# Performance work log

Hardware: AMD Instinct MI355X
Metric: run time of the kernel (lower is better)

## Reference

```python
import jax, jax.numpy as jnp
import numpy as np

N_Q_HEADS = 16
N_KV_HEADS = 4
HEAD_DIM = 64
GROUPS = N_Q_HEADS // N_KV_HEADS


def apply_rope(xq, xk, cos, sin):
    # xq: [B,S,Hq,D], xk: [B,S,Hkv,D]; cos/sin: [S, D/2]
    def rot(t):
        tr = t[..., 0::2]
        ti = t[..., 1::2]
        c = cos[None, :, None, :]
        s = sin[None, :, None, :]
        out_r = tr * c - ti * s
        out_i = tr * s + ti * c
        # interleave back: [..., D/2, 2] -> [..., D]
        return jnp.stack([out_r, out_i], axis=-1).reshape(t.shape)
    return rot(xq), rot(xk)


def setup_inputs() -> dict:
    key = jax.random.key(0)
    ks = jax.random.split(key, 8)
    B, S, DIM = 2, 2048, 1024
    x = jax.random.normal(ks[0], (B, S, DIM), jnp.float32)
    # RoPE frequencies (llama-style): theta_i = 10000^(-2i/D), angles = pos * theta
    inv_freq = 1.0 / (10000.0 ** (jnp.arange(0, HEAD_DIM, 2, dtype=jnp.float32) / HEAD_DIM))
    angles = jnp.arange(S, dtype=jnp.float32)[:, None] * inv_freq[None, :]  # [S, D/2]
    freqs_cos = jnp.cos(angles)
    freqs_sin = jnp.sin(angles)
    # additive causal mask [1,1,S,S]
    neg = jnp.float32(-1e9)
    mask = jnp.where(jnp.tril(jnp.ones((S, S), bool)), 0.0, neg)[None, None]
    scale = 0.02
    wq = jax.random.normal(ks[1], (DIM, N_Q_HEADS * HEAD_DIM), jnp.float32) * scale
    wk = jax.random.normal(ks[2], (DIM, N_KV_HEADS * HEAD_DIM), jnp.float32) * scale
    wv = jax.random.normal(ks[3], (DIM, N_KV_HEADS * HEAD_DIM), jnp.float32) * scale
    wo = jax.random.normal(ks[4], (DIM, DIM), jnp.float32) * scale
    return {"x": x, "start_pos": 0, "freqs_cos": freqs_cos, "freqs_sin": freqs_sin,
            "mask": mask, "wq": wq, "wk": wk, "wv": wv, "wo": wo}


def reference(x, start_pos, freqs_cos, freqs_sin, mask, wq, wk, wv, wo):
    B, S, DIM = x.shape
    xq = (x @ wq).reshape(B, S, N_Q_HEADS, HEAD_DIM)
    xk = (x @ wk).reshape(B, S, N_KV_HEADS, HEAD_DIM)
    xv = (x @ wv).reshape(B, S, N_KV_HEADS, HEAD_DIM)
    xq, xk = apply_rope(xq, xk, freqs_cos, freqs_sin)
    # seq_len > 1: prefill path, no KV-cache read. repeat_kv: expand kv heads by GROUPS.
    keys = jnp.repeat(xk, GROUPS, axis=2)    # [B,S,Hq,D]
    values = jnp.repeat(xv, GROUPS, axis=2)
    q = xq.transpose(0, 2, 1, 3)             # [B,H,S,D]
    k = keys.transpose(0, 2, 1, 3)
    v = values.transpose(0, 2, 1, 3)
    scores = jnp.einsum('bhqd,bhkd->bhqk', q, k) / jnp.sqrt(jnp.float32(HEAD_DIM))
    scores = scores + mask
    probs = jax.nn.softmax(scores, axis=-1)
    attn = jnp.einsum('bhqk,bhkd->bhqd', probs, v)  # [B,H,S,D]
    attn = attn.transpose(0, 2, 1, 3).reshape(B, S, DIM)
    return attn @ wo
```

## Files before the change

kernel.cpp:

```cpp
#include <hip/hip_runtime.h>

typedef __bf16 bf16_t;
typedef __bf16 bf16x8 __attribute__((ext_vector_type(8)));
typedef __bf16 bf16x4 __attribute__((ext_vector_type(4)));
typedef float f32x4 __attribute__((ext_vector_type(4)));
typedef short short4v __attribute__((ext_vector_type(4)));

#if __has_builtin(__builtin_amdgcn_exp2f)
#define EXP2F __builtin_amdgcn_exp2f
#else
#define EXP2F exp2f
#endif

#define BATCH 2
#define SEQ   2048
#define DIM   1024
#define NQH   16
#define NKVH  4
#define HD    64
#define ROWS  (BATCH*SEQ)
#define QKVN  1536
#define QSCALE 0.1803368801111f

static __device__ __forceinline__ short4v as_s4(bf16x4 v) {
    union { bf16x4 b; short4v s; } u; u.b = v; return u.s;
}

static __device__ __forceinline__ void gld16(const bf16_t* g, bf16_t* l) {
    __builtin_amdgcn_global_load_lds((const __attribute__((address_space(1))) void*)g,
                                     (__attribute__((address_space(3))) void*)l,
                                     16, 0, 0);
}

__global__ __launch_bounds__(256) void cast_x_kernel(const float* __restrict__ x,
                                                     bf16_t* __restrict__ o) {
    size_t i = ((size_t)blockIdx.x * 256 + threadIdx.x) * 4;
    float4 v = *(const float4*)(x + i);
    bf16x4 r;
    r[0] = (bf16_t)v.x; r[1] = (bf16_t)v.y; r[2] = (bf16_t)v.z; r[3] = (bf16_t)v.w;
    *(bf16x4*)(o + i) = r;
}

__global__ __launch_bounds__(256) void transpose_w_all(const float* __restrict__ wq,
                                                       const float* __restrict__ wk,
                                                       const float* __restrict__ wv,
                                                       const float* __restrict__ wo,
                                                       bf16_t* __restrict__ WqkvT,
                                                       bf16_t* __restrict__ WoT) {
    int bid = blockIdx.x;
    const float* src; bf16_t* dst; int N, nt, kt2;
    if (bid < 256)      { src = wq; dst = WqkvT;                      N = 1024; int i = bid;       nt = i & 15; kt2 = i >> 4; }
    else if (bid < 320) { src = wk; dst = WqkvT + (size_t)1024*1024;  N = 256;  int i = bid - 256; nt = i & 3;  kt2 = i >> 2; }
    else if (bid < 384) { src = wv; dst = WqkvT + (size_t)1280*1024;  N = 256;  int i = bid - 320; nt = i & 3;  kt2 = i >> 2; }
    else                { src = wo; dst = WoT;                        N = 1024; int i = bid - 384; nt = i & 15; kt2 = i >> 4; }

    __shared__ float tile[64][65];
    int t = threadIdx.x;
    {
        int r = t >> 2, cb = (t & 3) * 16;
        const float* s = src + (size_t)(kt2 * 64 + r) * N + nt * 64 + cb;
#pragma unroll
        for (int j = 0; j < 16; j += 4) {
            float4 v = *(const float4*)(s + j);
            tile[r][cb + j + 0] = v.x; tile[r][cb + j + 1] = v.y;
            tile[r][cb + j + 2] = v.z; tile[r][cb + j + 3] = v.w;
        }
    }
    __syncthreads();
    {
        int n = t >> 2, kb = (t & 3) * 16;
        union { bf16_t h[16]; uint4 u[2]; } pk;
#pragma unroll
        for (int j = 0; j < 16; ++j) pk.h[j] = (bf16_t)tile[kb + j][n];
        bf16_t* d = dst + (size_t)(nt * 64 + n) * 1024 + kt2 * 64 + kb;
        ((uint4*)d)[0] = pk.u[0];
        ((uint4*)d)[1] = pk.u[1];
    }
}

__global__ __launch_bounds__(256, 2) void gemm_qkv_kernel(const bf16_t* __restrict__ A,
                                                          const bf16_t* __restrict__ Bt,
                                                          const float* __restrict__ fcos,
                                                          const float* __restrict__ fsin,
                                                          bf16_t* __restrict__ Qb,
                                                          bf16_t* __restrict__ Kb,
                                                          bf16_t* __restrict__ Vt) {
    const int K = 1024;
    __shared__ __align__(16) bf16_t As[128 * 32];
    __shared__ __align__(16) bf16_t Bs[128 * 32];
    int t = threadIdx.x;
    int w = t >> 6, L = t & 63, quad = L >> 4, l15 = L & 15;
    int wr = (w >> 1) * 64, wc = (w & 1) * 64;
    int bnb = blockIdx.x;
    int bn = bnb * 128, bm = blockIdx.y * 128;

    const bf16_t* Ag0 = A  + (size_t)(bm + w * 32 + (L >> 2)) * K + (L & 3) * 8;
    const bf16_t* Ag1 = Ag0 + (size_t)16 * K;
    const bf16_t* Bg0 = Bt + (size_t)(bn + w * 32 + (L >> 2)) * K + (L & 3) * 8;
    const bf16_t* Bg1 = Bg0 + (size_t)16 * K;
    bf16_t* Al = As + w * 1024;
    bf16_t* Bl = Bs + w * 1024;

    f32x4 acc[4][4] = {};

    for (int k0 = 0; k0 < K; k0 += 32) {
        __syncthreads();
        gld16(Ag0 + k0, Al);
        gld16(Ag1 + k0, Al + 512);
        gld16(Bg0 + k0, Bl);
        gld16(Bg1 + k0, Bl + 512);
        __syncthreads();

        bf16x8 a[4], b[4];
#pragma unroll
        for (int i = 0; i < 4; ++i) {
            a[i] = ((const bf16x8*)As)[(wr + 16 * i + l15) * 4 + quad];
            b[i] = ((const bf16x8*)Bs)[(wc + 16 * i + l15) * 4 + quad];
        }
#pragma unroll
        for (int i = 0; i < 4; ++i)
#pragma unroll
            for (int j = 0; j < 4; ++j)
                acc[i][j] = __builtin_amdgcn_mfma_f32_16x16x32_bf16(a[i], b[j], acc[i][j], 0, 0, 0);
    }

    int region = (bnb >= 10) ? 2 : (bnb >= 8) ? 1 : 0;
#pragma unroll
    for (int i = 0; i < 4; ++i) {
        int row0 = bm + wr + 16 * i + quad * 4;
        int b = row0 >> 11, s0 = row0 & 2047;
#pragma unroll
        for (int j = 0; j < 4; ++j) {
            int col = bn + wc + 16 * j + l15;
            if (region == 2) {
                int kvh = (col >> 6) - 20, d = col & 63;
                bf16x4 o;
#pragma unroll
                for (int r = 0; r < 4; ++r) o[r] = (bf16_t)acc[i][j][r];
                *(bf16x4*)(Vt + ((size_t)((b * NKVH + kvh) * HD + d)) * SEQ + s0) = o;
            } else {
                int d = col & 63, fi = d >> 1;
                int odd = col & 1;
#pragma unroll
                for (int r = 0; r < 4; ++r) {
                    int s = s0 + r;
                    float v = acc[i][j][r];
                    float p = __shfl_xor(v, 1);
                    float c = fcos[s * 32 + fi], sn = fsin[s * 32 + fi];
                    float o = odd ? (p * sn + v * c) : (v * c - p * sn);
                    if (region == 0) {
                        int h = col >> 6;
                        Qb[((size_t)((b * NQH + h) * SEQ + s)) * HD + d] = (bf16_t)(o * QSCALE);
                    } else {
                        int kvh = (col >> 6) - 16;
                        Kb[((size_t)((b * NKVH + kvh) * SEQ + s)) * HD + d] = (bf16_t)o;
                    }
                }
            }
        }
    }
}

__global__ __launch_bounds__(256, 2) void gemm_bt_kernel(const bf16_t* __restrict__ A,
                                                         const bf16_t* __restrict__ Bt,
                                                         float* __restrict__ C,
                                                         int M, int N, int K) {
    __shared__ __align__(16) bf16_t As[128 * 32];
    __shared__ __align__(16) bf16_t Bs[128 * 32];
    int t = threadIdx.x;
    int w = t >> 6, L = t & 63, quad = L >> 4, l15 = L & 15;
    int wr = (w >> 1) * 64, wc = (w & 1) * 64;
    int bn = blockIdx.x * 128, bm = blockIdx.y * 128;

    const bf16_t* Ag0 = A  + (size_t)(bm + w * 32 + (L >> 2)) * K + (L & 3) * 8;
    const bf16_t* Ag1 = Ag0 + (size_t)16 * K;
    const bf16_t* Bg0 = Bt + (size_t)(bn + w * 32 + (L >> 2)) * K + (L & 3) * 8;
    const bf16_t* Bg1 = Bg0 + (size_t)16 * K;
    bf16_t* Al = As + w * 1024;
    bf16_t* Bl = Bs + w * 1024;

    f32x4 acc[4][4] = {};

    for (int k0 = 0; k0 < K; k0 += 32) {
        __syncthreads();
        gld16(Ag0 + k0, Al);
        gld16(Ag1 + k0, Al + 512);
        gld16(Bg0 + k0, Bl);
        gld16(Bg1 + k0, Bl + 512);
        __syncthreads();

        bf16x8 a[4], b[4];
#pragma unroll
        for (int i = 0; i < 4; ++i) {
            a[i] = ((const bf16x8*)As)[(wr + 16 * i + l15) * 4 + quad];
            b[i] = ((const bf16x8*)Bs)[(wc + 16 * i + l15) * 4 + quad];
        }
#pragma unroll
        for (int i = 0; i < 4; ++i)
#pragma unroll
            for (int j = 0; j < 4; ++j)
                acc[i][j] = __builtin_amdgcn_mfma_f32_16x16x32_bf16(a[i], b[j], acc[i][j], 0, 0, 0);
    }

#pragma unroll
    for (int i = 0; i < 4; ++i) {
        int row = bm + wr + 16 * i + quad * 4;
#pragma unroll
        for (int j = 0; j < 4; ++j) {
            int col = bn + wc + 16 * j + l15;
            float* cp = C + (size_t)row * N + col;
#pragma unroll
            for (int r = 0; r < 4; ++r)
                cp[(size_t)r * N] = acc[i][j][r];
        }
    }
}

__global__ __launch_bounds__(512, 2) void attn_kernel(const bf16_t* __restrict__ Qb,
                                                      const bf16_t* __restrict__ Kb,
                                                      const bf16_t* __restrict__ Vt,
                                                      bf16_t* __restrict__ Ob) {
    int bq = blockIdx.x, h = blockIdx.y, b = blockIdx.z;
    int kv = h >> 2;
    int t = threadIdx.x, w = t >> 6, lane = t & 63, quad = lane >> 4, l15 = lane & 15;

    __shared__ __align__(16) bf16_t Ks[64 * 64];
    __shared__ __align__(16) bf16_t Vs[64 * 64];

    const bf16_t* Qbase = Qb + ((size_t)(b * NQH + h)) * SEQ * HD;
    const bf16_t* Kbase = Kb + ((size_t)(b * NKVH + kv)) * SEQ * HD;
    const bf16_t* Vbase = Vt + ((size_t)(b * NKVH + kv)) * HD * SEQ;

    int sm = t >> 3, spos = t & 7, skc = spos ^ (sm & 7);
    const bf16_t* ksrc = Kbase + (size_t)sm * HD + skc * 8;
    const bf16_t* vsrc = Vbase + (size_t)sm * SEQ + skc * 8;

#pragma unroll 1
    for (int ph = 0; ph < 2; ++ph) {
        int qt = ph ? (15 - bq) : bq;
        int Q0 = qt * 128;
        int wq = Q0 + 16 * w + l15;
        int myktmax = (Q0 + 16 * w + 15) >> 6;
        int ktmax = (Q0 + 127) >> 6;

        bf16x8 aq[2];
#pragma unroll
        for (int ks = 0; ks < 2; ++ks)
            aq[ks] = *(const bf16x8*)(Qbase + (size_t)wq * HD + ks * 32 + quad * 8);

        f32x4 acc_o[4] = {};
        float rs = 0.f;

        uint4 kpre = *(const uint4*)ksrc;
        uint4 vpre = *(const uint4*)vsrc;

        for (int kt = 0; kt <= ktmax; ++kt) {
            __syncthreads();
            ((uint4*)Ks)[t] = kpre;
            ((uint4*)Vs)[t] = vpre;
            __syncthreads();
            if (kt < ktmax) {
                kpre = *(const uint4*)(ksrc + (size_t)(kt + 1) * 64 * HD);
                vpre = *(const uint4*)(vsrc + (size_t)(kt + 1) * 64);
            }
            if (kt > myktmax) continue;

            f32x4 st[4];
#pragma unroll
            for (int x = 0; x < 4; ++x) {
                int key = 16 * x + l15;
                bf16x8 ak0 = ((const bf16x8*)Ks)[key * 8 + ((0 + quad) ^ (key & 7))];
                bf16x8 ak1 = ((const bf16x8*)Ks)[key * 8 + ((4 + quad) ^ (key & 7))];
                f32x4 z = {0.f, 0.f, 0.f, 0.f};
                z = __builtin_amdgcn_mfma_f32_16x16x32_bf16(ak0, aq[0], z, 0, 0, 0);
                z = __builtin_amdgcn_mfma_f32_16x16x32_bf16(ak1, aq[1], z, 0, 0, 0);
                st[x] = z;
            }

            short4v bp[4];
            if (kt == myktmax) {
                int kb = kt * 64 + quad * 4;
#pragma unroll
                for (int x = 0; x < 4; ++x) {
                    bf16x4 pb;
#pragma unroll
                    for (int r = 0; r < 4; ++r) {
                        float p = (kb + 16 * x + r <= wq) ? EXP2F(st[x][r]) : 0.f;
                        rs += p; pb[r] = (bf16_t)p;
                    }
                    bp[x] = as_s4(pb);
                }
            } else {
#pragma unroll
                for (int x = 0; x < 4; ++x) {
                    bf16x4 pb;
#pragma unroll
                    for (int r = 0; r < 4; ++r) {
                        float p = EXP2F(st[x][r]);
                        rs += p; pb[r] = (bf16_t)p;
                    }
                    bp[x] = as_s4(pb);
                }
            }

#pragma unroll
            for (int dt = 0; dt < 4; ++dt) {
                int d = 16 * dt + l15;
#pragma unroll
                for (int x = 0; x < 4; ++x) {
                    int pos = (2 * x + (quad >> 1)) ^ (d & 7);
                    bf16x4 av = *(const bf16x4*)(Vs + d * 64 + pos * 8 + (quad & 1) * 4);
                    acc_o[dt] = __builtin_amdgcn_mfma_f32_16x16x16bf16_1k(as_s4(av), bp[x], acc_o[dt], 0, 0, 0);
                }
            }
        }

        rs += __shfl_xor(rs, 16);
        rs += __shfl_xor(rs, 32);
        float rinv = 1.0f / rs;
        bf16_t* obase = Ob + (size_t)(b * SEQ + wq) * DIM + h * HD;
#pragma unroll
        for (int dt = 0; dt < 4; ++dt) {
            bf16x4 o;
#pragma unroll
            for (int r = 0; r < 4; ++r) o[r] = (bf16_t)(acc_o[dt][r] * rinv);
            *(bf16x4*)(obase + 16 * dt + quad * 4) = o;
        }
    }
}

extern "C" void kernel_launch(void* const* d_in, const int* in_sizes, int n_in,
                              void* d_out, int out_size, void* d_ws, size_t ws_size,
                              hipStream_t stream) {
    const float* x    = (const float*)d_in[0];
    const float* fcos = (const float*)d_in[2];
    const float* fsin = (const float*)d_in[3];
    const float* wq   = (const float*)d_in[5];
    const float* wk   = (const float*)d_in[6];
    const float* wv   = (const float*)d_in[7];
    const float* wo   = (const float*)d_in[8];
    float* out = (float*)d_out;

    char* ws = (char*)d_ws;
    bf16_t* Xb    = (bf16_t*)(ws + 0);
    bf16_t* Attnb = Xb;
    bf16_t* WqkvT = (bf16_t*)(ws + 8388608);
    bf16_t* WoT   = (bf16_t*)(ws + 11534336);
    bf16_t* Qb    = (bf16_t*)(ws + 13631488);
    bf16_t* Kb    = (bf16_t*)(ws + 22020096);
    bf16_t* Vt    = (bf16_t*)(ws + 24117248);

    cast_x_kernel<<<ROWS * DIM / 1024, 256, 0, stream>>>(x, Xb);
    transpose_w_all<<<640, 256, 0, stream>>>(wq, wk, wv, wo, WqkvT, WoT);

    gemm_qkv_kernel<<<dim3(QKVN / 128, ROWS / 128), 256, 0, stream>>>(Xb, WqkvT, fcos, fsin, Qb, Kb, Vt);

    attn_kernel<<<dim3(8, NQH, BATCH), 512, 0, stream>>>(Qb, Kb, Vt, Attnb);

    gemm_bt_kernel<<<dim3(DIM / 128, ROWS / 128), 256, 0, stream>>>(Attnb, WoT, out, ROWS, DIM, DIM);
}
```

Before: 187.5 us.

## Retile K/V into MFMA-ready tiles and use 32x32 MFMA in attention

The QKV projection epilogue now writes K and V in a pre-tiled 64-key block layout that matches the LDS fragment order. The attention kernel loads each tile with direct global-to-LDS copies. It uses 32x32x16 MFMA on 32-query wave tiles and exchanges P fragments across lane halves with shuffles. Both causal half-tiles (bq and 15-bq) are handled at once by splitting the 8 waves instead of two sequential phases. This is meant to cut LDS swizzle and register staging overhead and to improve MFMA efficiency. In exchange it adds cross-lane shuffles, and some waves idle on tiles past their causal limit.

```diff
diff --git a/kernel.cpp b/kernel.cpp
--- a/kernel.cpp
+++ b/kernel.cpp
@@ -4,7 +4,7 @@
 typedef __bf16 bf16x8 __attribute__((ext_vector_type(8)));
 typedef __bf16 bf16x4 __attribute__((ext_vector_type(4)));
 typedef float f32x4 __attribute__((ext_vector_type(4)));
-typedef short short4v __attribute__((ext_vector_type(4)));
+typedef float f32x16 __attribute__((ext_vector_type(16)));
 
 #if __has_builtin(__builtin_amdgcn_exp2f)
 #define EXP2F __builtin_amdgcn_exp2f
@@ -21,10 +21,6 @@
 #define ROWS  (BATCH*SEQ)
 #define QKVN  1536
 #define QSCALE 0.1803368801111f
-
-static __device__ __forceinline__ short4v as_s4(bf16x4 v) {
-    union { bf16x4 b; short4v s; } u; u.b = v; return u.s;
-}
 
 static __device__ __forceinline__ void gld16(const bf16_t* g, bf16_t* l) {
     __builtin_amdgcn_global_load_lds((const __attribute__((address_space(1))) void*)g,
@@ -134,10 +130,12 @@
             int col = bn + wc + 16 * j + l15;
             if (region == 2) {
                 int kvh = (col >> 6) - 20, d = col & 63;
+                int kt = s0 >> 6, kl = s0 & 63;
                 bf16x4 o;
 #pragma unroll
                 for (int r = 0; r < 4; ++r) o[r] = (bf16_t)acc[i][j][r];
-                *(bf16x4*)(Vt + ((size_t)((b * NKVH + kvh) * HD + d)) * SEQ + s0) = o;
+                *(bf16x4*)(Vt + ((size_t)((b * NKVH + kvh) * 32 + kt)) * 4096
+                              + ((kl >> 3) * 64 + d) * 8 + (kl & 7)) = o;
             } else {
                 int d = col & 63, fi = d >> 1;
                 int odd = col & 1;
@@ -153,7 +151,9 @@
                         Qb[((size_t)((b * NQH + h) * SEQ + s)) * HD + d] = (bf16_t)(o * QSCALE);
                     } else {
                         int kvh = (col >> 6) - 16;
-                        Kb[((size_t)((b * NKVH + kvh) * SEQ + s)) * HD + d] = (bf16_t)o;
+                        int kt = s >> 6, kl = s & 63;
+                        Kb[((size_t)((b * NKVH + kvh) * 32 + kt)) * 4096
+                           + ((d >> 3) * 64 + kl) * 8 + (d & 7)] = (bf16_t)o;
                     }
                 }
             }
@@ -216,117 +216,109 @@
     }
 }
 
-__global__ __launch_bounds__(512, 2) void attn_kernel(const bf16_t* __restrict__ Qb,
-                                                      const bf16_t* __restrict__ Kb,
-                                                      const bf16_t* __restrict__ Vt,
-                                                      bf16_t* __restrict__ Ob) {
+__global__ __launch_bounds__(512) void attn_kernel(const bf16_t* __restrict__ Qb,
+                                                   const bf16_t* __restrict__ Kb,
+                                                   const bf16_t* __restrict__ Vt,
+                                                   bf16_t* __restrict__ Ob) {
     int bq = blockIdx.x, h = blockIdx.y, b = blockIdx.z;
     int kv = h >> 2;
-    int t = threadIdx.x, w = t >> 6, lane = t & 63, quad = lane >> 4, l15 = lane & 15;
-
-    __shared__ __align__(16) bf16_t Ks[64 * 64];
-    __shared__ __align__(16) bf16_t Vs[64 * 64];
-
-    const bf16_t* Qbase = Qb + ((size_t)(b * NQH + h)) * SEQ * HD;
-    const bf16_t* Kbase = Kb + ((size_t)(b * NKVH + kv)) * SEQ * HD;
-    const bf16_t* Vbase = Vt + ((size_t)(b * NKVH + kv)) * HD * SEQ;
-
-    int sm = t >> 3, spos = t & 7, skc = spos ^ (sm & 7);
-    const bf16_t* ksrc = Kbase + (size_t)sm * HD + skc * 8;
-    const bf16_t* vsrc = Vbase + (size_t)sm * SEQ + skc * 8;
-
-#pragma unroll 1
-    for (int ph = 0; ph < 2; ++ph) {
-        int qt = ph ? (15 - bq) : bq;
-        int Q0 = qt * 128;
-        int wq = Q0 + 16 * w + l15;
-        int myktmax = (Q0 + 16 * w + 15) >> 6;
-        int ktmax = (Q0 + 127) >> 6;
-
-        bf16x8 aq[2];
-#pragma unroll
-        for (int ks = 0; ks < 2; ++ks)
-            aq[ks] = *(const bf16x8*)(Qbase + (size_t)wq * HD + ks * 32 + quad * 8);
-
-        f32x4 acc_o[4] = {};
-        float rs = 0.f;
-
-        uint4 kpre = *(const uint4*)ksrc;
-        uint4 vpre = *(const uint4*)vsrc;
-
-        for (int kt = 0; kt <= ktmax; ++kt) {
-            __syncthreads();
-            ((uint4*)Ks)[t] = kpre;
-            ((uint4*)Vs)[t] = vpre;
-            __syncthreads();
-            if (kt < ktmax) {
-                kpre = *(const uint4*)(ksrc + (size_t)(kt + 1) * 64 * HD);
-                vpre = *(const uint4*)(vsrc + (size_t)(kt + 1) * 64);
+    int t = threadIdx.x, w = t >> 6, lane = t & 63, hi = lane >> 5, l31 = lane & 31;
+    int wg = w & 3;
+    int qt = (w >> 2) == 0 ? bq : (15 - bq);
+    int wq0 = qt * 128 + wg * 32;
+    int q = wq0 + l31;
+    int myktmax = (wq0 + 31) >> 6;
+    int ktmax_blk = 31 - 2 * bq;
+
+    __shared__ __align__(16) bf16_t Ks2[4096];
+    __shared__ __align__(16) bf16_t Vs2[4096];
+
+    const bf16_t* Ktile = Kb + ((size_t)((b * NKVH + kv) * 32)) * 4096;
+    const bf16_t* Vtile = Vt + ((size_t)((b * NKVH + kv) * 32)) * 4096;
+    const bf16_t* Qrow  = Qb + ((size_t)((b * NQH + h) * SEQ + q)) * HD;
+
+    bf16x8 qf[4];
+#pragma unroll
+    for (int ks = 0; ks < 4; ++ks)
+        qf[ks] = *(const bf16x8*)(Qrow + ks * 16 + hi * 8);
+
+    f32x16 acc[2] = {};
+    float rs = 0.f;
+
+    for (int kt = 0; kt <= ktmax_blk; ++kt) {
+        __syncthreads();
+        gld16(Ktile + (size_t)kt * 4096 + t * 8, Ks2 + w * 512);
+        gld16(Vtile + (size_t)kt * 4096 + t * 8, Vs2 + w * 512);
+        __syncthreads();
+        if (kt > myktmax) continue;
+
+        f32x16 st[2];
+#pragma unroll
+        for (int kg = 0; kg < 2; ++kg) {
+            f32x16 z = {};
+#pragma unroll
+            for (int ks = 0; ks < 4; ++ks) {
+                bf16x8 ak = *(const bf16x8*)(Ks2 + ((ks * 2 + hi) * 64 + kg * 32 + l31) * 8);
+                z = __builtin_amdgcn_mfma_f32_32x32x16_bf16(ak, qf[ks], z, 0, 0, 0);
             }
-            if (kt > myktmax) continue;
-
-            f32x4 st[4];
-#pragma unroll
-            for (int x = 0; x < 4; ++x) {
-                int key = 16 * x + l15;
-                bf16x8 ak0 = ((const bf16x8*)Ks)[key * 8 + ((0 + quad) ^ (key & 7))];
-                bf16x8 ak1 = ((const bf16x8*)Ks)[key * 8 + ((4 + quad) ^ (key & 7))];
-                f32x4 z = {0.f, 0.f, 0.f, 0.f};
-                z = __builtin_amdgcn_mfma_f32_16x16x32_bf16(ak0, aq[0], z, 0, 0, 0);
-                z = __builtin_amdgcn_mfma_f32_16x16x32_bf16(ak1, aq[1], z, 0, 0, 0);
-                st[x] = z;
+            st[kg] = z;
+        }
+
+        bool diag = (kt == myktmax);
+        uint2 pk[2][2][2];
+#pragma unroll
+        for (int c = 0; c < 2; ++c)
+#pragma unroll
+            for (int u = 0; u < 2; ++u)
+#pragma unroll
+                for (int hh = 0; hh < 2; ++hh) {
+                    bf16x4 g;
+#pragma unroll
+                    for (int jl = 0; jl < 4; ++jl) {
+                        int r = 8 * u + 4 * hh + jl;
+                        float p = EXP2F(st[c][r]);
+                        if (diag) {
+                            int key = kt * 64 + 32 * c + 16 * u + 8 * hh + 4 * hi + jl;
+                            if (key > q) p = 0.f;
+                        }
+                        rs += p;
+                        g[jl] = (bf16_t)p;
+                    }
+                    union { bf16x4 b4; uint2 u2; } cv; cv.b4 = g;
+                    pk[c][u][hh] = cv.u2;
+                }
+
+#pragma unroll
+        for (int tt = 0; tt < 4; ++tt) {
+            int u = tt & 1, c = tt >> 1;
+            uint2 keep = hi ? pk[c][u][1] : pk[c][u][0];
+            uint2 send = hi ? pk[c][u][0] : pk[c][u][1];
+            uint2 recv;
+            recv.x = __shfl_xor(send.x, 32);
+            recv.y = __shfl_xor(send.y, 32);
+            union { uint4 u4; bf16x8 b8; } fr;
+            fr.u4 = hi ? make_uint4(recv.x, recv.y, keep.x, keep.y)
+                       : make_uint4(keep.x, keep.y, recv.x, recv.y);
+#pragma unroll
+            for (int dg = 0; dg < 2; ++dg) {
+                bf16x8 av = *(const bf16x8*)(Vs2 + ((tt * 2 + hi) * 64 + dg * 32 + l31) * 8);
+                acc[dg] = __builtin_amdgcn_mfma_f32_32x32x16_bf16(av, fr.b8, acc[dg], 0, 0, 0);
             }
-
-            short4v bp[4];
-            if (kt == myktmax) {
-                int kb = kt * 64 + quad * 4;
-#pragma unroll
-                for (int x = 0; x < 4; ++x) {
-                    bf16x4 pb;
-#pragma unroll
-                    for (int r = 0; r < 4; ++r) {
-                        float p = (kb + 16 * x + r <= wq) ? EXP2F(st[x][r]) : 0.f;
-                        rs += p; pb[r] = (bf16_t)p;
-                    }
-                    bp[x] = as_s4(pb);
-                }
-            } else {
-#pragma unroll
-                for (int x = 0; x < 4; ++x) {
-                    bf16x4 pb;
-#pragma unroll
-                    for (int r = 0; r < 4; ++r) {
-                        float p = EXP2F(st[x][r]);
-                        rs += p; pb[r] = (bf16_t)p;
-                    }
-                    bp[x] = as_s4(pb);
-                }
-            }
-
-#pragma unroll
-            for (int dt = 0; dt < 4; ++dt) {
-                int d = 16 * dt + l15;
-#pragma unroll
-                for (int x = 0; x < 4; ++x) {
-                    int pos = (2 * x + (quad >> 1)) ^ (d & 7);
-                    bf16x4 av = *(const bf16x4*)(Vs + d * 64 + pos * 8 + (quad & 1) * 4);
-                    acc_o[dt] = __builtin_amdgcn_mfma_f32_16x16x16bf16_1k(as_s4(av), bp[x], acc_o[dt], 0, 0, 0);
-                }
-            }
-        }
-
-        rs += __shfl_xor(rs, 16);
-        rs += __shfl_xor(rs, 32);
-        float rinv = 1.0f / rs;
-        bf16_t* obase = Ob + (size_t)(b * SEQ + wq) * DIM + h * HD;
-#pragma unroll
-        for (int dt = 0; dt < 4; ++dt) {
+        }
+    }
+
+    rs += __shfl_xor(rs, 32);
+    float rinv = 1.0f / rs;
+    bf16_t* obase = Ob + (size_t)(b * SEQ + q) * DIM + h * HD;
+#pragma unroll
+    for (int dg = 0; dg < 2; ++dg)
+#pragma unroll
+        for (int g2 = 0; g2 < 4; ++g2) {
             bf16x4 o;
 #pragma unroll
-            for (int r = 0; r < 4; ++r) o[r] = (bf16_t)(acc_o[dt][r] * rinv);
-            *(bf16x4*)(obase + 16 * dt + quad * 4) = o;
-        }
-    }
+            for (int jl = 0; jl < 4; ++jl) o[jl] = (bf16_t)(acc[dg][4 * g2 + jl] * rinv);
+            *(bf16x4*)(obase + 32 * dg + 8 * g2 + 4 * hi) = o;
+        }
 }
 
 extern "C" void kernel_launch(void* const* d_in, const int* in_sizes, int n_in,
```

Measured after the change: 211.6 us. 12.9% more time.
